# Performance work log

Measured on AMD Instinct MI355X. Metric: run time of the kernel, lower is better.

The kernel has to match this reference:

```python
import jax, jax.numpy as jnp
import numpy as np

SEARCH_RANGE = 4  # matches init_kwargs


def setup_inputs() -> dict:
    key = jax.random.key(0)
    k1, k2 = jax.random.split(key)
    shape = (8, 256, 64, 128)  # [B, C, H, W]
    feature1 = jax.random.normal(k1, shape, dtype=jnp.float32)
    feature2 = jax.random.normal(k2, shape, dtype=jnp.float32)
    return {"feature1": feature1, "feature2": feature2}


def reference(feature1, feature2):
    R = SEARCH_RANGE
    b, c, h, w = feature1.shape
    # zero-pad feature2 spatially by R on each side
    f2p = jnp.pad(feature2, ((0, 0), (0, 0), (R, R), (R, R)))
    D = 2 * R + 1
    # shift offsets in the same order as the original nested loop (idx outer, jdx inner)
    offsets = jnp.stack(
        jnp.meshgrid(jnp.arange(D), jnp.arange(D), indexing="ij"), axis=-1
    ).reshape(-1, 2)  # [81, 2]

    def corr_one(ij):
        win = jax.lax.dynamic_slice(f2p, (0, 0, ij[0], ij[1]), (b, c, h, w))
        return jnp.sum(feature1 * win, axis=1)  # [B, H, W]

    dots = jax.vmap(corr_one)(offsets)  # [81, B, H, W]
    return jnp.transpose(dots, (1, 0, 2, 3))  # [B, 81, H, W]
```

## Files before the change

kernel.cpp:

```cpp
#include <hip/hip_runtime.h>
#include <cstdint>

typedef __attribute__((ext_vector_type(8))) short short8;
typedef __attribute__((ext_vector_type(4))) float floatx4;
typedef __attribute__((ext_vector_type(2))) unsigned int uintx2;
typedef __attribute__((ext_vector_type(4))) unsigned int uintx4;

__device__ __forceinline__ uint32_t pack2(float a, float b) {
    uint32_t ua = __builtin_bit_cast(uint32_t, a);
    uint32_t ub = __builtin_bit_cast(uint32_t, b);
    ua = (ua + 0x7FFFu + ((ua >> 16) & 1u)) >> 16;
    ub = (ub + 0x7FFFu + ((ub >> 16) & 1u)) >> 16;
    return ua | (ub << 16);
}

#define CC_SLAB  ((size_t)8 * 64 * 2304)
#define T2P_WORDS (8 * CC_SLAB)
#define WS_NEED   (T2P_WORDS * 4 + 4096)

__global__ __launch_bounds__(256)
void transpose_f2(const float* __restrict__ f2, uint32_t* __restrict__ t2p) {
    __shared__ float t[64][33];
    const int tid = threadIdx.x;
    const int bid = blockIdx.x;
    const int b = bid & 7, h = (bid >> 3) & 63, wt = bid >> 9;
    const int w0 = wt * 32;
    const float* f2b = f2 + (size_t)b * 256 * 8192 + (size_t)h * 128 + w0;

    const int rw = tid & 31, rc8 = tid >> 5;
    const int tp = tid & 127, rr = tid >> 7;
    const int m  = tp & 15;

    for (int cc = 0; cc < 4; ++cc) {
        if (cc) __syncthreads();
#pragma unroll
        for (int i = 0; i < 8; ++i)
            t[rc8 * 8 + i][rw] = f2b[(size_t)(cc * 64 + rc8 * 8 + i) * 8192 + rw];
        __syncthreads();
        const int cc2 = 2 * cc + rr;
        uint32_t* dst = t2p + (size_t)cc2 * CC_SLAB
                        + ((size_t)b * 64 + h) * 2304 + (size_t)(w0 + 4) * 16;
#pragma unroll
        for (int i = 0; i < 4; ++i) {
            int d = i * 128 + tp;
            int j = d >> 4;
            dst[d] = pack2(t[rr * 32 + 2 * m][j], t[rr * 32 + 2 * m + 1][j]);
        }
    }
    if (wt == 0) {
        for (int idx = tid; idx < 512; idx += 256) {
            int cc2 = idx >> 6, o = idx & 63;
            t2p[(size_t)cc2 * CC_SLAB + ((size_t)b * 64 + h) * 2304 + o] = 0;
        }
    }
    if (wt == 3) {
        for (int idx = tid; idx < 1536; idx += 256) {
            int cc2 = idx / 192, o = idx % 192;
            t2p[(size_t)cc2 * CC_SLAB + ((size_t)b * 64 + h) * 2304 + 132 * 16 + o] = 0;
        }
    }
    if (bid == 0) {
        uint32_t* z = t2p + T2P_WORDS;
        for (int idx = tid; idx < 1024; idx += 256) z[idx] = 0;
    }
}

#define AS1 __attribute__((address_space(1)))
#define AS3 __attribute__((address_space(3)))

__device__ __forceinline__ void gld_lds16(const uint32_t* src, uint32_t* dst) {
    __builtin_amdgcn_global_load_lds((const AS1 void*)src, (AS3 void*)dst, 16, 0, 0);
}

#define BUF_WORDS 9216
#define DUMP_OFF  (4 * BUF_WORDS)

__global__ __launch_bounds__(1024, 4)
void corr3(const float* __restrict__ f1, const uint32_t* __restrict__ t2p,
           const uint32_t* __restrict__ wsZ, float* __restrict__ out) {
    __shared__ uint32_t ldsB[4 * BUF_WORDS + 256];

    const int tid  = threadIdx.x;
    const int lane = tid & 63;
    const int wh   = tid >> 6;
    const int n15  = lane & 15;
    const int q    = lane >> 4;

    const int bid = blockIdx.x;
    const int b  = bid & 7;
    const int ht = (bid >> 3) & 3;
    const int wt = bid >> 5;
    const int h0 = 16 * ht, w0 = 16 * wt;
    const int h  = h0 + wh;
    const int p  = b;

    const float* f1b = f1 + (size_t)b * 256 * 8192;

    uint32_t bOff[3], ccMul[3];
    int bOffL[3];
    bool dumpf[3];
#pragma unroll
    for (int s = 0; s < 3; ++s) {
        int sg = wh * 3 + s;
        bool dummy = (sg & 3) == 3;
        int rank = (sg >> 2) * 3 + (sg & 3);
        int f = rank * 16 + (lane >> 2);
        int r = f / 24, cidx = f % 24;
        int gh = h0 - 4 + r;
        int gd = (lane & 3) ^ ((cidx >> 1) & 3);
        bool inb = !dummy && ((unsigned)gh < 64u);
        bOff[s]  = inb ? (uint32_t)((b * 64 + gh) * 2304 + (w0 + cidx) * 16 + gd * 4)
                       : (uint32_t)(T2P_WORDS + lane * 4);
        ccMul[s] = inb ? (uint32_t)CC_SLAB : 0u;
        bOffL[s] = rank * 256;
        dumpf[s] = dummy;
    }

    const float* aBase = f1b + (size_t)h * 128 + w0 + n15;

    floatx4 acc[9][2];
#pragma unroll
    for (int di = 0; di < 9; ++di)
#pragma unroll
        for (int t = 0; t < 2; ++t)
            acc[di][t] = (floatx4){0.f, 0.f, 0.f, 0.f};

    const int rdB = n15 * 16 + ((q ^ ((n15 >> 1) & 3)) << 2);

    auto stageB = [&](int bufsel, int cc) {
        uint32_t* dbase = ldsB + bufsel * BUF_WORDS;
#pragma unroll
        for (int s = 0; s < 3; ++s) {
            const uint32_t* src = t2p + (size_t)(bOff[s] + (uint32_t)cc * ccMul[s]);
            uint32_t* d = dumpf[s] ? (ldsB + DUMP_OFF) : (dbase + bOffL[s]);
            gld_lds16(src, d);
        }
    };
    auto loadA = [&](float* r, int cc) {
        const float* ap = aBase + (size_t)(32 * cc + 8 * q) * 8192;
#pragma unroll
        for (int j = 0; j < 8; ++j) r[j] = ap[(size_t)j * 8192];
    };
    auto packA = [&](const float* r) -> short8 {
        uintx4 av = {pack2(r[0], r[1]), pack2(r[2], r[3]),
                     pack2(r[4], r[5]), pack2(r[6], r[7])};
        return __builtin_bit_cast(short8, av);
    };
    auto mfma9 = [&](int bufsel, short8 a0) {
        const uint32_t* bufB = ldsB + bufsel * BUF_WORDS;
#pragma unroll
        for (int di = 0; di < 9; ++di) {
            const uint32_t* p0 = bufB + (wh + di) * 384 + rdB;
            uintx4 v0 = *(const uintx4*)p0;
            uintx4 v1 = *(const uintx4*)(p0 + 128);
            short8 b0 = __builtin_bit_cast(short8, v0);
            short8 b1 = __builtin_bit_cast(short8, v1);
            acc[di][0] = __builtin_amdgcn_mfma_f32_16x16x32_bf16(a0, b0, acc[di][0], 0, 0, 0);
            acc[di][1] = __builtin_amdgcn_mfma_f32_16x16x32_bf16(a0, b1, acc[di][1], 0, 0, 0);
        }
    };

    float rA0[8], rA1[8];
#define ROT(t) (((t) + p) & 7)
#define SB __builtin_amdgcn_sched_barrier(0)

    loadA(rA0, ROT(0)); SB;
    stageB(0, ROT(0)); SB;
    loadA(rA1, ROT(1)); SB;
    stageB(1, ROT(1)); SB;
    stageB(2, ROT(2)); SB;

#define CHUNK(K, VM, RS)                                                      \
    {                                                                         \
        asm volatile("s_waitcnt vmcnt(" #VM ")\n\ts_barrier" ::: "memory");   \
        short8 a0 = packA(RS);                                                \
        SB;                                                                   \
        if ((K) <= 5) loadA(RS, ROT((K) + 2));                                \
        SB;                                                                   \
        if ((K) <= 4) stageB(((K) + 3) & 3, ROT((K) + 3));                    \
        SB;                                                                   \
        mfma9((K) & 3, a0);                                                   \
    }

    CHUNK(0, 14, rA0)
    CHUNK(1, 14, rA1)
    CHUNK(2, 14, rA0)
    CHUNK(3, 14, rA1)
    CHUNK(4, 14, rA0)
    CHUNK(5, 14, rA1)
    CHUNK(6, 11, rA0)
    CHUNK(7, 0,  rA1)
#undef CHUNK
#undef ROT
#undef SB

    const size_t base = ((size_t)b * 81) * 8192 + (size_t)h * 128 + w0;
#pragma unroll
    for (int di = 0; di < 9; ++di) {
#pragma unroll
        for (int t = 0; t < 2; ++t) {
#pragma unroll
            for (int r = 0; r < 4; ++r) {
                int mp = 4 * q + r;
                int dj = t * 8 + n15 - mp;
                if (dj >= 0 && dj <= 8 && (t == 0 || n15 >= 8)) {
                    out[base + (size_t)(di * 9 + dj) * 8192 + mp] = acc[di][t][r];
                }
            }
        }
    }
}

#define CS 18
#define A_WORDS (8 * 16 * CS)
#define B_ROWS  13
#define B_WORDS (B_ROWS * 24 * CS)

__device__ __forceinline__ short8 frag_ld(const uint32_t* p) {
    uintx2 lo = *(const uintx2*)p;
    uintx2 hi = *(const uintx2*)(p + 2);
    uintx4 v = {lo.x, lo.y, hi.x, hi.y};
    return __builtin_bit_cast(short8, v);
}

__global__ __launch_bounds__(512, 4)
void corr_kernel(const float* __restrict__ f1, const float* __restrict__ f2,
                 float* __restrict__ out) {
    __shared__ uint32_t ldsA[2 * A_WORDS];
    __shared__ uint32_t ldsB2[2 * B_WORDS];

    const int tid  = threadIdx.x;
    const int lane = tid & 63;
    const int wh   = tid >> 6;
    const int n15  = lane & 15;
    const int q    = lane >> 4;

    const int bid    = blockIdx.x;
    const int b      = bid & 7;
    const int dihalf = (bid >> 3) & 1;
    const int ht     = (bid >> 4) & 7;
    const int wt     = bid >> 7;

    const int w0 = wt * 16;
    const int h0 = ht * 8;
    const int h  = h0 + wh;

    const int diN    = dihalf ? 4 : 5;
    const int diBase = dihalf * 5;
    const int ghBase = dihalf ? (h0 + 1) : (h0 - 4);

    const float* f1b = f1 + (size_t)b * 256 * 8192;
    const float* f2b = f2 + (size_t)b * 256 * 8192;

    const int aw4 = tid & 3, akp = (tid >> 2) & 15, arow = tid >> 6;
    int aOffG = (2 * akp) * 8192 + (h0 + arow) * 128 + (w0 + 4 * aw4);
    const int aLds = (arow * 16 + 4 * aw4) * CS + akp;

    int bOffG[3]; int bLds[3]; uint32_t bMask[3];
#pragma unroll
    for (int s = 0; s < 3; ++s) {
        int t = tid + 512 * s;
        int w4 = t % 6;
        int r2 = t / 6;
        int kp = r2 & 15, row = r2 >> 4;
        int gh = ghBase + row;
        int gw = w0 - 4 + 4 * w4;
        bool live = (t < 1152);
        bool inb  = live && ((unsigned)gh < 64u) && ((unsigned)gw < 128u);
        bOffG[s] = inb ? ((2 * kp) * 8192 + gh * 128 + gw) : 0;
        bLds[s]  = live ? ((row * 24 + 4 * w4) * CS + kp) : ((12 * 24 + (tid & 7)) * CS);
        bMask[s] = inb ? 0xFFFFFFFFu : 0u;
    }

    floatx4 acc[5][2];
#pragma unroll
    for (int dl = 0; dl < 5; ++dl)
#pragma unroll
        for (int t = 0; t < 2; ++t)
            acc[dl][t] = (floatx4){0.f, 0.f, 0.f, 0.f};

    floatx4 rA[2], rB[3][2];
    uint32_t pkA[4], pkB[12];

    auto issue = [&]() {
        rA[0] = *(const floatx4*)(f1b + aOffG);
        rA[1] = *(const floatx4*)(f1b + aOffG + 8192);
        aOffG += 32 * 8192;
#pragma unroll
        for (int s = 0; s < 3; ++s) {
            rB[s][0] = *(const floatx4*)(f2b + bOffG[s]);
            rB[s][1] = *(const floatx4*)(f2b + bOffG[s] + 8192);
            bOffG[s] += 32 * 8192;
        }
    };
    auto packall = [&]() {
#pragma unroll
        for (int i = 0; i < 4; ++i) pkA[i] = pack2(rA[0][i], rA[1][i]);
#pragma unroll
        for (int s = 0; s < 3; ++s)
#pragma unroll
            for (int i = 0; i < 4; ++i)
                pkB[4 * s + i] = pack2(rB[s][0][i], rB[s][1][i]) & bMask[s];
    };

    issue(); packall();

    for (int ch = 0; ch < 8; ++ch) {
        uint32_t* bufA = ldsA + (ch & 1) * A_WORDS;
        uint32_t* bufB = ldsB2 + (ch & 1) * B_WORDS;
#pragma unroll
        for (int i = 0; i < 4; ++i) bufA[aLds + i * CS] = pkA[i];
#pragma unroll
        for (int s = 0; s < 3; ++s)
#pragma unroll
            for (int i = 0; i < 4; ++i) bufB[bLds[s] + i * CS] = pkB[4 * s + i];
        if (ch < 7) issue();
        __syncthreads();

        const uint32_t* pa = bufA + (wh * 16 + n15) * CS + 4 * q;
        short8 a0 = frag_ld(pa);
        const uint32_t* pb = bufB + (wh * 24 + n15) * CS + 4 * q;
#pragma unroll
        for (int dl = 0; dl < 5; ++dl) {
            if (dl < diN) {
                const uint32_t* pp = pb + dl * (24 * CS);
                short8 b0 = frag_ld(pp);
                short8 b1 = frag_ld(pp + 8 * CS);
                acc[dl][0] = __builtin_amdgcn_mfma_f32_16x16x32_bf16(a0, b0, acc[dl][0], 0, 0, 0);
                acc[dl][1] = __builtin_amdgcn_mfma_f32_16x16x32_bf16(a0, b1, acc[dl][1], 0, 0, 0);
            }
        }
        if (ch < 7) packall();
    }

    const size_t base = ((size_t)b * 81) * 8192 + (size_t)h * 128 + w0;
#pragma unroll
    for (int dl = 0; dl < 5; ++dl) {
        if (dl < diN) {
            const int dio = diBase + dl;
#pragma unroll
            for (int t = 0; t < 2; ++t) {
#pragma unroll
                for (int r = 0; r < 4; ++r) {
                    int mp = 4 * q + r;
                    int dj = t * 8 + n15 - mp;
                    if (dj >= 0 && dj <= 8 && (t == 0 || n15 >= 8)) {
                        out[base + (size_t)(dio * 9 + dj) * 8192 + mp] = acc[dl][t][r];
                    }
                }
            }
        }
    }
}

extern "C" void kernel_launch(void* const* d_in, const int* in_sizes, int n_in,
                              void* d_out, int out_size, void* d_ws, size_t ws_size,
                              hipStream_t stream) {
    const float* f1 = (const float*)d_in[0];
    const float* f2 = (const float*)d_in[1];
    float* out = (float*)d_out;
    if (ws_size >= WS_NEED && d_ws != nullptr) {
        uint32_t* t2p = (uint32_t*)d_ws;
        transpose_f2<<<dim3(2048), dim3(256), 0, stream>>>(f2, t2p);
        corr3<<<dim3(256), dim3(1024), 0, stream>>>(f1, t2p, t2p + T2P_WORDS, out);
    } else {
        corr_kernel<<<dim3(1024), dim3(512), 0, stream>>>(f1, f2, out);
    }
}
```

Measured before the change: 179.8 us.

## Double channel-chunk size per pipeline stage with two-buffer LDS pipeline

Each pipeline step now processes 64 channels instead of 32. It stages two half-buffers of B into LDS and loads 16 A values per lane, which doubles the MFMAs issued between barriers. The ring goes from four 32-channel buffers to two 64-channel buffers, with the same total LDS, and the loop drops from 8 to 4 chunks. This halves the barrier and waitcnt synchronisation count but gives shallower prefetch depth and more A-register pressure.

```diff
diff --git a/kernel.cpp b/kernel.cpp
--- a/kernel.cpp
+++ b/kernel.cpp
@@ -72,13 +72,14 @@
     __builtin_amdgcn_global_load_lds((const AS1 void*)src, (AS3 void*)dst, 16, 0, 0);
 }
 
-#define BUF_WORDS 9216
-#define DUMP_OFF  (4 * BUF_WORDS)
+#define HBUF_WORDS 9216
+#define CBUF_WORDS (2 * HBUF_WORDS)
+#define DUMP_OFF   (2 * CBUF_WORDS)
 
 __global__ __launch_bounds__(1024, 4)
-void corr3(const float* __restrict__ f1, const uint32_t* __restrict__ t2p,
+void corr4(const float* __restrict__ f1, const uint32_t* __restrict__ t2p,
            const uint32_t* __restrict__ wsZ, float* __restrict__ out) {
-    __shared__ uint32_t ldsB[4 * BUF_WORDS + 256];
+    __shared__ uint32_t ldsB[2 * CBUF_WORDS + 256];
 
     const int tid  = threadIdx.x;
     const int lane = tid & 63;
@@ -92,7 +93,7 @@
     const int wt = bid >> 5;
     const int h0 = 16 * ht, w0 = 16 * wt;
     const int h  = h0 + wh;
-    const int p  = b;
+    const int p4 = b & 3;
 
     const float* f1b = f1 + (size_t)b * 256 * 8192;
 
@@ -128,70 +129,79 @@
     const int rdB = n15 * 16 + ((q ^ ((n15 >> 1) & 3)) << 2);
 
     auto stageB = [&](int bufsel, int cc) {
-        uint32_t* dbase = ldsB + bufsel * BUF_WORDS;
-#pragma unroll
-        for (int s = 0; s < 3; ++s) {
-            const uint32_t* src = t2p + (size_t)(bOff[s] + (uint32_t)cc * ccMul[s]);
-            uint32_t* d = dumpf[s] ? (ldsB + DUMP_OFF) : (dbase + bOffL[s]);
-            gld_lds16(src, d);
+        uint32_t* dbase = ldsB + bufsel * CBUF_WORDS;
+#pragma unroll
+        for (int half = 0; half < 2; ++half) {
+#pragma unroll
+            for (int s = 0; s < 3; ++s) {
+                const uint32_t* src = t2p + (size_t)(bOff[s] + (uint32_t)(2 * cc + half) * ccMul[s]);
+                uint32_t* d = dumpf[s] ? (ldsB + DUMP_OFF) : (dbase + half * HBUF_WORDS + bOffL[s]);
+                gld_lds16(src, d);
+            }
         }
     };
     auto loadA = [&](float* r, int cc) {
-        const float* ap = aBase + (size_t)(32 * cc + 8 * q) * 8192;
-#pragma unroll
-        for (int j = 0; j < 8; ++j) r[j] = ap[(size_t)j * 8192];
+        const float* a0p = aBase + (size_t)(64 * cc + 8 * q) * 8192;
+        const float* a1p = aBase + (size_t)(64 * cc + 32 + 8 * q) * 8192;
+#pragma unroll
+        for (int j = 0; j < 8; ++j) r[j] = a0p[(size_t)j * 8192];
+#pragma unroll
+        for (int j = 0; j < 8; ++j) r[8 + j] = a1p[(size_t)j * 8192];
     };
     auto packA = [&](const float* r) -> short8 {
         uintx4 av = {pack2(r[0], r[1]), pack2(r[2], r[3]),
                      pack2(r[4], r[5]), pack2(r[6], r[7])};
         return __builtin_bit_cast(short8, av);
     };
-    auto mfma9 = [&](int bufsel, short8 a0) {
-        const uint32_t* bufB = ldsB + bufsel * BUF_WORDS;
+    auto mfma36 = [&](int bufsel, short8 a0, short8 a1) {
+        const uint32_t* bh0 = ldsB + bufsel * CBUF_WORDS;
+        const uint32_t* bh1 = bh0 + HBUF_WORDS;
 #pragma unroll
         for (int di = 0; di < 9; ++di) {
-            const uint32_t* p0 = bufB + (wh + di) * 384 + rdB;
+            const uint32_t* p0 = bh0 + (wh + di) * 384 + rdB;
             uintx4 v0 = *(const uintx4*)p0;
             uintx4 v1 = *(const uintx4*)(p0 + 128);
-            short8 b0 = __builtin_bit_cast(short8, v0);
-            short8 b1 = __builtin_bit_cast(short8, v1);
-            acc[di][0] = __builtin_amdgcn_mfma_f32_16x16x32_bf16(a0, b0, acc[di][0], 0, 0, 0);
-            acc[di][1] = __builtin_amdgcn_mfma_f32_16x16x32_bf16(a0, b1, acc[di][1], 0, 0, 0);
-        }
-    };
-
-    float rA0[8], rA1[8];
-#define ROT(t) (((t) + p) & 7)
+            acc[di][0] = __builtin_amdgcn_mfma_f32_16x16x32_bf16(
+                a0, __builtin_bit_cast(short8, v0), acc[di][0], 0, 0, 0);
+            acc[di][1] = __builtin_amdgcn_mfma_f32_16x16x32_bf16(
+                a0, __builtin_bit_cast(short8, v1), acc[di][1], 0, 0, 0);
+            const uint32_t* p1 = bh1 + (wh + di) * 384 + rdB;
+            uintx4 w0v = *(const uintx4*)p1;
+            uintx4 w1v = *(const uintx4*)(p1 + 128);
+            acc[di][0] = __builtin_amdgcn_mfma_f32_16x16x32_bf16(
+                a1, __builtin_bit_cast(short8, w0v), acc[di][0], 0, 0, 0);
+            acc[di][1] = __builtin_amdgcn_mfma_f32_16x16x32_bf16(
+                a1, __builtin_bit_cast(short8, w1v), acc[di][1], 0, 0, 0);
+        }
+    };
+
+    float rA0[16], rA1[16];
+#define ROT4(t) (((t) + p4) & 3)
 #define SB __builtin_amdgcn_sched_barrier(0)
 
-    loadA(rA0, ROT(0)); SB;
-    stageB(0, ROT(0)); SB;
-    loadA(rA1, ROT(1)); SB;
-    stageB(1, ROT(1)); SB;
-    stageB(2, ROT(2)); SB;
+    loadA(rA0, ROT4(0)); SB;
+    stageB(0, ROT4(0)); SB;
+    loadA(rA1, ROT4(1)); SB;
 
 #define CHUNK(K, VM, RS)                                                      \
     {                                                                         \
         asm volatile("s_waitcnt vmcnt(" #VM ")\n\ts_barrier" ::: "memory");   \
         short8 a0 = packA(RS);                                                \
+        short8 a1 = packA(RS + 8);                                            \
         SB;                                                                   \
-        if ((K) <= 5) loadA(RS, ROT((K) + 2));                                \
+        if ((K) <= 2) stageB(((K) + 1) & 1, ROT4((K) + 1));                   \
         SB;                                                                   \
-        if ((K) <= 4) stageB(((K) + 3) & 3, ROT((K) + 3));                    \
+        if ((K) <= 1) loadA(RS, ROT4((K) + 2));                               \
         SB;                                                                   \
-        mfma9((K) & 3, a0);                                                   \
-    }
-
-    CHUNK(0, 14, rA0)
-    CHUNK(1, 14, rA1)
-    CHUNK(2, 14, rA0)
-    CHUNK(3, 14, rA1)
-    CHUNK(4, 14, rA0)
-    CHUNK(5, 14, rA1)
-    CHUNK(6, 11, rA0)
-    CHUNK(7, 0,  rA1)
+        mfma36((K) & 1, a0, a1);                                              \
+    }
+
+    CHUNK(0, 16, rA0)
+    CHUNK(1, 16, rA1)
+    CHUNK(2, 16, rA0)
+    CHUNK(3, 0,  rA1)
 #undef CHUNK
-#undef ROT
+#undef ROT4
 #undef SB
 
     const size_t base = ((size_t)b * 81) * 8192 + (size_t)h * 128 + w0;
@@ -362,7 +372,7 @@
     if (ws_size >= WS_NEED && d_ws != nullptr) {
         uint32_t* t2p = (uint32_t*)d_ws;
         transpose_f2<<<dim3(2048), dim3(256), 0, stream>>>(f2, t2p);
-        corr3<<<dim3(256), dim3(1024), 0, stream>>>(f1, t2p, t2p + T2P_WORDS, out);
+        corr4<<<dim3(256), dim3(1024), 0, stream>>>(f1, t2p, t2p + T2P_WORDS, out);
     } else {
         corr_kernel<<<dim3(1024), dim3(512), 0, stream>>>(f1, f2, out);
     }
```

New measurement: 181.7 us. About the same (+1.1%).
